# Kernel optimization log

Measured on AMD Instinct MI355X. Metric: run time of the kernel, lower is better.

The kernel has to match this reference:

```python
import jax, jax.numpy as jnp
import numpy as np

N, E, G = 20000, 400000, 200
IN, HID, OUT, H = 8, 64, 32, 4
EPS = 1e-5
NEG_SLOPE = 0.2


def _gatv2(x, src, dst, Wl, bl, Wr, br, att, bias, n, heads, c):
    # lin_l (source messages) and lin_r (target queries)
    xl = (x @ Wl + bl).reshape(n, heads, c)
    xr = (x @ Wr + br).reshape(n, heads, c)
    # per-edge GATv2 score: att . LeakyReLU(x_l[j] + x_r[i])
    e = jax.nn.leaky_relu(xl[src] + xr[dst], NEG_SLOPE)          # [E,H,C]
    score = jnp.einsum('ehc,hc->eh', e, att)                     # [E,H]
    # softmax over incoming edges of each target node
    m = jax.ops.segment_max(score, dst, num_segments=n)
    ex = jnp.exp(score - m[dst])
    den = jax.ops.segment_sum(ex, dst, num_segments=n)
    alpha = ex / den[dst]                                        # [E,H]
    out = jax.ops.segment_sum(alpha[:, :, None] * xl[src], dst, num_segments=n)
    return out.mean(axis=1) + bias                               # concat=False: head mean


def _layernorm(x, g, b):
    mu = x.mean(-1, keepdims=True)
    var = ((x - mu) ** 2).mean(-1, keepdims=True)
    return (x - mu) * jax.lax.rsqrt(var + EPS) * g + b


def setup_inputs() -> dict:
    key = jax.random.key(0)
    ks = jax.random.split(key, 16)
    s = 0.1
    inp = {
        'x': jax.random.normal(ks[0], (N, IN), jnp.float32),
        'edge_index': jax.random.randint(ks[1], (2, E), 0, N, jnp.int64 if jax.config.jax_enable_x64 else jnp.int32),
        'batch': jnp.sort(jax.random.randint(ks[2], (N,), 0, G)),
        'Wl1': jax.random.normal(ks[3], (IN, H * HID), jnp.float32) * s,
        'bl1': jnp.zeros((H * HID,), jnp.float32),
        'Wr1': jax.random.normal(ks[4], (IN, H * HID), jnp.float32) * s,
        'br1': jnp.zeros((H * HID,), jnp.float32),
        'att1': jax.random.normal(ks[5], (H, HID), jnp.float32) * s,
        'b1': jnp.zeros((HID,), jnp.float32),
        'ln1_g': jnp.ones((HID,), jnp.float32),
        'ln1_b': jnp.zeros((HID,), jnp.float32),
        'Wl2': jax.random.normal(ks[6], (HID, H * OUT), jnp.float32) * s,
        'bl2': jnp.zeros((H * OUT,), jnp.float32),
        'Wr2': jax.random.normal(ks[7], (HID, H * OUT), jnp.float32) * s,
        'br2': jnp.zeros((H * OUT,), jnp.float32),
        'att2': jax.random.normal(ks[8], (H, OUT), jnp.float32) * s,
        'b2': jnp.zeros((OUT,), jnp.float32),
        'ln2_g': jnp.ones((OUT,), jnp.float32),
        'ln2_b': jnp.zeros((OUT,), jnp.float32),
    }
    return inp


def reference(x, edge_index, batch, Wl1, bl1, Wr1, br1, att1, b1, ln1_g, ln1_b,
              Wl2, bl2, Wr2, br2, att2, b2, ln2_g, ln2_b):
    n = x.shape[0]
    loop = jnp.arange(n, dtype=edge_index.dtype)  # add_self_loops=True (PyG default)
    src = jnp.concatenate([edge_index[0], loop])
    dst = jnp.concatenate([edge_index[1], loop])

    h = _gatv2(x, src, dst, Wl1, bl1, Wr1, br1, att1, b1, n, H, HID)
    h = jax.nn.relu(_layernorm(h, ln1_g, ln1_b))
    h = _gatv2(h, src, dst, Wl2, bl2, Wr2, br2, att2, b2, n, H, OUT)
    h = jax.nn.relu(_layernorm(h, ln2_g, ln2_b))

    # global mean pool per graph
    cnt = jax.ops.segment_sum(jnp.ones((n,), h.dtype), batch, num_segments=G)
    pooled = jax.ops.segment_sum(h, batch, num_segments=G)
    return pooled / jnp.maximum(cnt, 1.0)[:, None]
```

## Files before the change

kernel.cpp:

```cpp
#include <hip/hip_runtime.h>
#include <math.h>
#include <stdint.h>

#define NEG_SLOPE 0.2f
#define LN_EPS 1e-5f

typedef __attribute__((ext_vector_type(8))) short short8;
typedef __attribute__((ext_vector_type(4))) float f32x4;

__device__ __forceinline__ uint32_t pack_bf2(float a, float b) {
  uint32_t ua = __float_as_uint(a);
  uint32_t ub = __float_as_uint(b);
  ua = (ua + 0x7fffu + ((ua >> 16) & 1u)) >> 16;
  ub = (ub + 0x7fffu + ((ub >> 16) & 1u)) & 0xffff0000u;
  return ua | ub;
}
__device__ __forceinline__ float2 unpack_bf2(uint32_t u) {
  return make_float2(__uint_as_float(u << 16), __uint_as_float(u & 0xffff0000u));
}
__device__ __forceinline__ uint16_t bf16_rne(float f) {
  uint32_t u = __float_as_uint(f);
  return (uint16_t)((u + 0x7fffu + ((u >> 16) & 1u)) >> 16);
}

__device__ __forceinline__ float row16_sum(float x) {
  x += __int_as_float(__builtin_amdgcn_mov_dpp(__float_as_int(x), 0xB1, 0xF, 0xF, true));
  x += __int_as_float(__builtin_amdgcn_mov_dpp(__float_as_int(x), 0x4E, 0xF, 0xF, true));
  x += __int_as_float(__builtin_amdgcn_mov_dpp(__float_as_int(x), 0x124, 0xF, 0xF, true));
  x += __int_as_float(__builtin_amdgcn_mov_dpp(__float_as_int(x), 0x128, 0xF, 0xF, true));
  return x;
}

__global__ __launch_bounds__(256) void gemm1_hist_kernel(
    const float* __restrict__ x,
    const float* __restrict__ Wl, const float* __restrict__ bl,
    const float* __restrict__ Wr, const float* __restrict__ br,
    uint32_t* __restrict__ xl1b, float* __restrict__ xr1, int N,
    const int* __restrict__ ei, int E, int* __restrict__ cnt) {
  int tid = threadIdx.x;
  int c2 = tid & 127;
  int which = tid >> 7;
  float wl0[8], wl1[8], wr0[8], wr1[8];
#pragma unroll
  for (int k = 0; k < 8; ++k) {
    wl0[k] = Wl[k * 256 + 2 * c2]; wl1[k] = Wl[k * 256 + 2 * c2 + 1];
    wr0[k] = Wr[k * 256 + 2 * c2]; wr1[k] = Wr[k * 256 + 2 * c2 + 1];
  }
  float bl0 = bl[2 * c2], bl1v = bl[2 * c2 + 1];
  float br0 = br[2 * c2], br1v = br[2 * c2 + 1];
  int npair = (N + 1) >> 1;
  for (int pr = blockIdx.x; pr < npair; pr += gridDim.x) {
    int n = pr * 2 + which;
    if (n >= N) continue;
    float4 xa = ((const float4*)x)[n * 2];
    float4 xb = ((const float4*)x)[n * 2 + 1];
    float xs[8] = {xa.x, xa.y, xa.z, xa.w, xb.x, xb.y, xb.z, xb.w};
    float al0 = bl0, al1 = bl1v, ar0 = br0, ar1 = br1v;
#pragma unroll
    for (int k = 0; k < 8; ++k) {
      al0 = fmaf(xs[k], wl0[k], al0); al1 = fmaf(xs[k], wl1[k], al1);
      ar0 = fmaf(xs[k], wr0[k], ar0); ar1 = fmaf(xs[k], wr1[k], ar1);
    }
    xl1b[(size_t)n * 128 + c2] = pack_bf2(al0, al1);
    ((float2*)xr1)[(size_t)n * 128 + c2] = make_float2(ar0, ar1);
  }
  int tot = E + N;
  for (int e = blockIdx.x * blockDim.x + tid; e < tot; e += gridDim.x * blockDim.x) {
    int dst = (e < E) ? ei[E + e] : (e - E);
    atomicAdd(&cnt[dst], 1);
  }
}

__global__ __launch_bounds__(1024) void scan_kernel(const int* __restrict__ cnt,
                                                    int* __restrict__ offs,
                                                    int* __restrict__ cursor, int n) {
  __shared__ int wsum[16];
  int tid = threadIdx.x;
  int lane = tid & 63, w = tid >> 6;
  int PER = (n + 1023) >> 10;
  int base = tid * PER;
  int s = 0;
  for (int j = 0; j < PER; ++j) {
    int idx = base + j;
    s += (idx < n) ? cnt[idx] : 0;
  }
  int inc = s;
#pragma unroll
  for (int d = 1; d < 64; d <<= 1) {
    int t = __shfl_up(inc, d, 64);
    if (lane >= d) inc += t;
  }
  if (lane == 63) wsum[w] = inc;
  __syncthreads();
  int wpre = 0;
  for (int j = 0; j < w; ++j) wpre += wsum[j];
  int run = wpre + inc - s;
  for (int j = 0; j < PER; ++j) {
    int idx = base + j;
    if (idx < n) {
      offs[idx] = run;
      cursor[idx] = run;
      run += cnt[idx];
    }
  }
  if (tid == 1023) offs[n] = run;
}

__global__ void scatter_kernel(const int* __restrict__ ei, int E, int N,
                               int* __restrict__ cursor, int* __restrict__ esrc,
                               const float* __restrict__ Wl2, const float* __restrict__ Wr2,
                               uint16_t* __restrict__ Wtb) {
  if (blockIdx.x < 64) {
    int idx = blockIdx.x * 256 + threadIdx.x;
    int c = idx >> 6, k = idx & 63;
    float v = (c < 128) ? Wl2[k * 128 + c] : Wr2[k * 128 + (c - 128)];
    Wtb[idx] = bf16_rne(v);
  }
  int e = blockIdx.x * blockDim.x + threadIdx.x;
  if (e >= E + N) return;
  int src, dst;
  if (e < E) { src = ei[e]; dst = ei[E + e]; }
  else       { src = e - E; dst = src; }
  int pos = atomicAdd(&cursor[dst], 1);
  esrc[pos] = src;
}

__global__ __launch_bounds__(256) void gemm2_mfma_kernel(
    const uint16_t* __restrict__ h1b,
    const uint16_t* __restrict__ Wtb,
    const float* __restrict__ bl, const float* __restrict__ br,
    uint32_t* __restrict__ xl2b, float* __restrict__ xr2, int N) {
  int lane = threadIdx.x & 63;
  int w = threadIdx.x >> 6;
  int c0 = w << 6;
  int l15 = lane & 15, l4 = lane >> 4;
  int node = (blockIdx.x << 4) + l15;
  int nodec = node < N ? node : N - 1;
  const short8* hrow = (const short8*)(h1b + (size_t)nodec * 64);
  short8 b0 = hrow[l4];
  short8 b1 = hrow[4 + l4];
  f32x4 acc[4] = {{0.f,0.f,0.f,0.f},{0.f,0.f,0.f,0.f},{0.f,0.f,0.f,0.f},{0.f,0.f,0.f,0.f}};
#pragma unroll
  for (int t = 0; t < 4; ++t) {
    int row = c0 + (t << 4) + l15;
    const short8* wrow = (const short8*)(Wtb + (size_t)row * 64);
    short8 a0 = wrow[l4];
    short8 a1 = wrow[4 + l4];
    acc[t] = __builtin_amdgcn_mfma_f32_16x16x32_bf16(a0, b0, acc[t], 0, 0, 0);
    acc[t] = __builtin_amdgcn_mfma_f32_16x16x32_bf16(a1, b1, acc[t], 0, 0, 0);
  }
  if (node >= N) return;
  if (c0 < 128) {
#pragma unroll
    for (int t = 0; t < 4; ++t) {
      int q0 = c0 + (t << 4) + (l4 << 2);
      float4 bb = *(const float4*)(bl + q0);
      uint2 pk;
      pk.x = pack_bf2(acc[t][0] + bb.x, acc[t][1] + bb.y);
      pk.y = pack_bf2(acc[t][2] + bb.z, acc[t][3] + bb.w);
      *(uint2*)(xl2b + (size_t)node * 64 + (q0 >> 1)) = pk;
    }
  } else {
#pragma unroll
    for (int t = 0; t < 4; ++t) {
      int q0 = (c0 - 128) + (t << 4) + (l4 << 2);
      float4 bb = *(const float4*)(br + q0);
      float4 v = make_float4(acc[t][0] + bb.x, acc[t][1] + bb.y,
                             acc[t][2] + bb.z, acc[t][3] + bb.w);
      *(float4*)(xr2 + (size_t)node * 128 + q0) = v;
    }
  }
}

__global__ __launch_bounds__(256) void attn1_kernel(
    const uint32_t* __restrict__ xl1b, const float* __restrict__ xr1,
    const float* __restrict__ att, const float* __restrict__ b1,
    const float* __restrict__ g, const float* __restrict__ be,
    const int* __restrict__ offs, const int* __restrict__ esrc,
    uint32_t* __restrict__ h1b, int N) {
  int lane = threadIdx.x & 63;
  int i = blockIdx.x * (blockDim.x >> 6) + (threadIdx.x >> 6);
  if (i >= N) return;
  int cq = lane & 15;
  const uint2* xlb = (const uint2*)xl1b;
  float4 attq = ((const float4*)att)[lane];
  float4 attn_ = make_float4(NEG_SLOPE * attq.x, NEG_SLOPE * attq.y,
                             NEG_SLOPE * attq.z, NEG_SLOPE * attq.w);
  float4 xrq = ((const float4*)xr1)[(size_t)i * 64 + lane];
  float dA = 0.f, aA0 = 0.f, aA1 = 0.f, aA2 = 0.f, aA3 = 0.f;
  float dB = 0.f, aB0 = 0.f, aB1 = 0.f, aB2 = 0.f, aB3 = 0.f;
  int beg = offs[i], end = offs[i + 1];
  int p = beg;

#define EDGE1(U, DD, A0, A1, A2, A3)                                           \
  {                                                                            \
    float2 e0 = unpack_bf2(U.x), e1 = unpack_bf2(U.y);                         \
    float t0 = e0.x + xrq.x, t1 = e0.y + xrq.y;                                \
    float t2 = e1.x + xrq.z, t3 = e1.y + xrq.w;                                \
    float sc = t0 * (t0 > 0.f ? attq.x : attn_.x);                             \
    sc = fmaf(t1, (t1 > 0.f ? attq.y : attn_.y), sc);                          \
    sc = fmaf(t2, (t2 > 0.f ? attq.z : attn_.z), sc);                          \
    sc = fmaf(t3, (t3 > 0.f ? attq.w : attn_.w), sc);                          \
    sc = row16_sum(sc);                                                        \
    float wgt = __expf(sc);                                                    \
    DD += wgt;                                                                 \
    A0 = fmaf(wgt, e0.x, A0); A1 = fmaf(wgt, e0.y, A1);                        \
    A2 = fmaf(wgt, e1.x, A2); A3 = fmaf(wgt, e1.y, A3);                        \
  }

  for (; p + 3 < end; p += 4) {
    int s0 = esrc[p], s1 = esrc[p + 1], s2 = esrc[p + 2], s3 = esrc[p + 3];
    uint2 u0 = xlb[(uint32_t)s0 * 64u + lane];
    uint2 u1 = xlb[(uint32_t)s1 * 64u + lane];
    uint2 u2 = xlb[(uint32_t)s2 * 64u + lane];
    uint2 u3 = xlb[(uint32_t)s3 * 64u + lane];
    EDGE1(u0, dA, aA0, aA1, aA2, aA3)
    EDGE1(u1, dB, aB0, aB1, aB2, aB3)
    EDGE1(u2, dA, aA0, aA1, aA2, aA3)
    EDGE1(u3, dB, aB0, aB1, aB2, aB3)
  }
  for (; p < end; ++p) {
    int s0 = esrc[p];
    uint2 u0 = xlb[(uint32_t)s0 * 64u + lane];
    EDGE1(u0, dA, aA0, aA1, aA2, aA3)
  }
#undef EDGE1

  float inv = 1.0f / (dA + dB);
  float v0 = (aA0 + aB0) * inv;
  float v1 = (aA1 + aB1) * inv;
  float v2 = (aA2 + aB2) * inv;
  float v3 = (aA3 + aB3) * inv;
  v0 += __shfl_xor(v0, 16, 64); v0 += __shfl_xor(v0, 32, 64);
  v1 += __shfl_xor(v1, 16, 64); v1 += __shfl_xor(v1, 32, 64);
  v2 += __shfl_xor(v2, 16, 64); v2 += __shfl_xor(v2, 32, 64);
  v3 += __shfl_xor(v3, 16, 64); v3 += __shfl_xor(v3, 32, 64);
  float4 b1q = ((const float4*)b1)[cq];
  v0 = 0.25f * v0 + b1q.x;
  v1 = 0.25f * v1 + b1q.y;
  v2 = 0.25f * v2 + b1q.z;
  v3 = 0.25f * v3 + b1q.w;
  float s1 = row16_sum(v0 + v1 + v2 + v3);
  float mu = s1 * (1.0f / 64.0f);
  float d0 = v0 - mu, d1 = v1 - mu, d2 = v2 - mu, d3 = v3 - mu;
  float s2 = row16_sum(d0 * d0 + d1 * d1 + d2 * d2 + d3 * d3);
  float rstd = rsqrtf(s2 * (1.0f / 64.0f) + LN_EPS);
  float4 gq = ((const float4*)g)[cq];
  float4 beq = ((const float4*)be)[cq];
  float y0 = fmaxf(fmaf(d0 * rstd, gq.x, beq.x), 0.f);
  float y1 = fmaxf(fmaf(d1 * rstd, gq.y, beq.y), 0.f);
  float y2 = fmaxf(fmaf(d2 * rstd, gq.z, beq.z), 0.f);
  float y3 = fmaxf(fmaf(d3 * rstd, gq.w, beq.w), 0.f);
  if (lane < 16) {
    uint2 pk;
    pk.x = pack_bf2(y0, y1);
    pk.y = pack_bf2(y2, y3);
    *(uint2*)(h1b + (size_t)i * 32 + cq * 2) = pk;
  }
}

__global__ __launch_bounds__(256) void attn2_kernel(
    const uint32_t* __restrict__ xl2b, const float* __restrict__ xr2,
    const float* __restrict__ att, const float* __restrict__ b2,
    const float* __restrict__ g, const float* __restrict__ be,
    const int* __restrict__ offs, const int* __restrict__ esrc,
    float* __restrict__ h2, int N) {
  int lane = threadIdx.x & 63;
  int i = blockIdx.x * (blockDim.x >> 6) + (threadIdx.x >> 6);
  if (i >= N) return;
  int cq = lane & 15;
  float2 attq = ((const float2*)att)[lane];
  float2 attn_ = make_float2(NEG_SLOPE * attq.x, NEG_SLOPE * attq.y);
  float2 xrq = ((const float2*)xr2)[(size_t)i * 64 + lane];
  float dA = 0.f, aA0 = 0.f, aA1 = 0.f;
  float dB = 0.f, aB0 = 0.f, aB1 = 0.f;
  int beg = offs[i], end = offs[i + 1];
  int p = beg;

#define EDGE2(U, DD, A0, A1)                                                   \
  {                                                                            \
    float2 e0 = unpack_bf2(U);                                                 \
    float t0 = e0.x + xrq.x, t1 = e0.y + xrq.y;                                \
    float sc = t0 * (t0 > 0.f ? attq.x : attn_.x);                             \
    sc = fmaf(t1, (t1 > 0.f ? attq.y : attn_.y), sc);                          \
    sc = row16_sum(sc);                                                        \
    float wgt = __expf(sc);                                                    \
    DD += wgt;                                                                 \
    A0 = fmaf(wgt, e0.x, A0); A1 = fmaf(wgt, e0.y, A1);                        \
  }

  for (; p + 3 < end; p += 4) {
    int s0 = esrc[p], s1 = esrc[p + 1], s2 = esrc[p + 2], s3 = esrc[p + 3];
    uint32_t u0 = xl2b[(uint32_t)s0 * 64u + lane];
    uint32_t u1 = xl2b[(uint32_t)s1 * 64u + lane];
    uint32_t u2 = xl2b[(uint32_t)s2 * 64u + lane];
    uint32_t u3 = xl2b[(uint32_t)s3 * 64u + lane];
    EDGE2(u0, dA, aA0, aA1)
    EDGE2(u1, dB, aB0, aB1)
    EDGE2(u2, dA, aA0, aA1)
    EDGE2(u3, dB, aB0, aB1)
  }
  for (; p < end; ++p) {
    int s0 = esrc[p];
    uint32_t u0 = xl2b[(uint32_t)s0 * 64u + lane];
    EDGE2(u0, dA, aA0, aA1)
  }
#undef EDGE2

  float inv = 1.0f / (dA + dB);
  float v0 = (aA0 + aB0) * inv;
  float v1 = (aA1 + aB1) * inv;
  v0 += __shfl_xor(v0, 16, 64); v0 += __shfl_xor(v0, 32, 64);
  v1 += __shfl_xor(v1, 16, 64); v1 += __shfl_xor(v1, 32, 64);
  float2 b2q = ((const float2*)b2)[cq];
  v0 = 0.25f * v0 + b2q.x;
  v1 = 0.25f * v1 + b2q.y;
  float s1 = row16_sum(v0 + v1);
  float mu = s1 * (1.0f / 32.0f);
  float d0 = v0 - mu, d1 = v1 - mu;
  float s2 = row16_sum(d0 * d0 + d1 * d1);
  float rstd = rsqrtf(s2 * (1.0f / 32.0f) + LN_EPS);
  float2 gq = ((const float2*)g)[cq];
  float2 beq = ((const float2*)be)[cq];
  float y0 = fmaxf(fmaf(d0 * rstd, gq.x, beq.x), 0.f);
  float y1 = fmaxf(fmaf(d1 * rstd, gq.y, beq.y), 0.f);
  if (lane < 16) ((float2*)h2)[(size_t)i * 16 + cq] = make_float2(y0, y1);
}

__global__ __launch_bounds__(256) void pool_kernel(const float* __restrict__ h2,
                                                   const int* __restrict__ batch,
                                                   float* __restrict__ out, int N) {
  int gidx = blockIdx.x;
  int a = 0, b = N;
  while (a < b) { int m = (a + b) >> 1; if (batch[m] < gidx) a = m + 1; else b = m; }
  int lo = a;
  b = N;
  while (a < b) { int m = (a + b) >> 1; if (batch[m] < gidx + 1) a = m + 1; else b = m; }
  int hi = a;
  int c = threadIdx.x & 31, r = threadIdx.x >> 5;
  float s = 0.f;
  for (int n = lo + r; n < hi; n += 8) s += h2[(size_t)n * 32 + c];
  __shared__ float buf[256];
  buf[threadIdx.x] = s;
  __syncthreads();
  if (threadIdx.x < 128) buf[threadIdx.x] += buf[threadIdx.x + 128];
  __syncthreads();
  if (threadIdx.x < 64) buf[threadIdx.x] += buf[threadIdx.x + 64];
  __syncthreads();
  if (threadIdx.x < 32) {
    float v = buf[threadIdx.x] + buf[threadIdx.x + 32];
    int cnt = hi - lo;
    out[gidx * 32 + threadIdx.x] = v / (float)(cnt > 0 ? cnt : 1);
  }
}

extern "C" void kernel_launch(void* const* d_in, const int* in_sizes, int n_in,
                              void* d_out, int out_size, void* d_ws, size_t ws_size,
                              hipStream_t stream) {
  const float* x    = (const float*)d_in[0];
  const int*   ei   = (const int*)d_in[1];
  const int*   batch= (const int*)d_in[2];
  const float* Wl1  = (const float*)d_in[3];
  const float* bl1  = (const float*)d_in[4];
  const float* Wr1  = (const float*)d_in[5];
  const float* br1  = (const float*)d_in[6];
  const float* att1 = (const float*)d_in[7];
  const float* b1   = (const float*)d_in[8];
  const float* ln1g = (const float*)d_in[9];
  const float* ln1b = (const float*)d_in[10];
  const float* Wl2  = (const float*)d_in[11];
  const float* bl2  = (const float*)d_in[12];
  const float* Wr2  = (const float*)d_in[13];
  const float* br2  = (const float*)d_in[14];
  const float* att2 = (const float*)d_in[15];
  const float* b2   = (const float*)d_in[16];
  const float* ln2g = (const float*)d_in[17];
  const float* ln2b = (const float*)d_in[18];

  int N = in_sizes[0] / 8;
  int E = in_sizes[1] / 2;
  int G = out_size / 32;

  char* ws = (char*)d_ws;
  size_t off = 0;
  auto alloc = [&](size_t bytes) -> void* {
    void* p = (void*)(ws + off);
    off += (bytes + 255) & ~(size_t)255;
    return p;
  };
  int*      cnt    = (int*)alloc((size_t)N * 4);
  int*      offs   = (int*)alloc((size_t)(N + 1) * 4);
  int*      cursor = (int*)alloc((size_t)N * 4);
  int*      esrc   = (int*)alloc((size_t)(E + N) * 4);
  uint32_t* xl1b   = (uint32_t*)alloc((size_t)N * 128 * 4);
  float*    xr1    = (float*)alloc((size_t)N * 256 * 4);
  uint32_t* h1b    = (uint32_t*)alloc((size_t)N * 64 * 2);
  uint16_t* Wtb    = (uint16_t*)alloc((size_t)256 * 64 * 2);
  uint32_t* xl2b   = (uint32_t*)alloc((size_t)N * 64 * 4);
  float*    xr2    = (float*)alloc((size_t)N * 128 * 4);
  float*    h2     = (float*)alloc((size_t)N * 32 * 4);

  hipMemsetAsync(cnt, 0, (size_t)N * 4, stream);

  int tot = E + N;
  gemm1_hist_kernel<<<2048, 256, 0, stream>>>(x, Wl1, bl1, Wr1, br1, xl1b, xr1, N,
                                              ei, E, cnt);
  scan_kernel<<<1, 1024, 0, stream>>>(cnt, offs, cursor, N);
  scatter_kernel<<<(tot + 255) / 256, 256, 0, stream>>>(ei, E, N, cursor, esrc,
                                                        Wl2, Wr2, Wtb);

  attn1_kernel<<<(N + 3) / 4, 256, 0, stream>>>(xl1b, xr1, att1, b1, ln1g, ln1b,
                                                offs, esrc, h1b, N);
  gemm2_mfma_kernel<<<(N + 15) / 16, 256, 0, stream>>>((const uint16_t*)h1b, Wtb, bl2, br2,
                                                       xl2b, xr2, N);
  attn2_kernel<<<(N + 3) / 4, 256, 0, stream>>>(xl2b, xr2, att2, b2, ln2g, ln2b,
                                                offs, esrc, h2, N);

  pool_kernel<<<G, 256, 0, stream>>>(h2, batch, (float*)d_out, N);
}
```

Before: 173.6 us.

## Use abs-based LeakyReLU with exp2, scalarize edge indices, replace memset with kernel

```diff
diff --git a/kernel.cpp b/kernel.cpp
--- a/kernel.cpp
+++ b/kernel.cpp
@@ -29,6 +29,11 @@
   x += __int_as_float(__builtin_amdgcn_mov_dpp(__float_as_int(x), 0x124, 0xF, 0xF, true));
   x += __int_as_float(__builtin_amdgcn_mov_dpp(__float_as_int(x), 0x128, 0xF, 0xF, true));
   return x;
+}
+
+__global__ void zero_kernel(int* __restrict__ p, int n) {
+  int i = blockIdx.x * blockDim.x + threadIdx.x;
+  if (i < n) p[i] = 0;
 }
 
 __global__ __launch_bounds__(256) void gemm1_hist_kernel(
@@ -178,14 +183,15 @@
     const float* __restrict__ g, const float* __restrict__ be,
     const int* __restrict__ offs, const int* __restrict__ esrc,
     uint32_t* __restrict__ h1b, int N) {
+  const float L2E = 1.4426950408889634f;
   int lane = threadIdx.x & 63;
   int i = blockIdx.x * (blockDim.x >> 6) + (threadIdx.x >> 6);
   if (i >= N) return;
   int cq = lane & 15;
   const uint2* xlb = (const uint2*)xl1b;
   float4 attq = ((const float4*)att)[lane];
-  float4 attn_ = make_float4(NEG_SLOPE * attq.x, NEG_SLOPE * attq.y,
-                             NEG_SLOPE * attq.z, NEG_SLOPE * attq.w);
+  float4 a4 = make_float4(0.4f * L2E * attq.x, 0.4f * L2E * attq.y,
+                          0.4f * L2E * attq.z, 0.4f * L2E * attq.w);
   float4 xrq = ((const float4*)xr1)[(size_t)i * 64 + lane];
   float dA = 0.f, aA0 = 0.f, aA1 = 0.f, aA2 = 0.f, aA3 = 0.f;
   float dB = 0.f, aB0 = 0.f, aB1 = 0.f, aB2 = 0.f, aB3 = 0.f;
@@ -197,31 +203,38 @@
     float2 e0 = unpack_bf2(U.x), e1 = unpack_bf2(U.y);                         \
     float t0 = e0.x + xrq.x, t1 = e0.y + xrq.y;                                \
     float t2 = e1.x + xrq.z, t3 = e1.y + xrq.w;                                \
-    float sc = t0 * (t0 > 0.f ? attq.x : attn_.x);                             \
-    sc = fmaf(t1, (t1 > 0.f ? attq.y : attn_.y), sc);                          \
-    sc = fmaf(t2, (t2 > 0.f ? attq.z : attn_.z), sc);                          \
-    sc = fmaf(t3, (t3 > 0.f ? attq.w : attn_.w), sc);                          \
+    float u0 = fmaf(1.5f, t0, fabsf(t0));                                      \
+    float u1 = fmaf(1.5f, t1, fabsf(t1));                                      \
+    float u2 = fmaf(1.5f, t2, fabsf(t2));                                      \
+    float u3 = fmaf(1.5f, t3, fabsf(t3));                                      \
+    float sc = a4.x * u0;                                                      \
+    sc = fmaf(a4.y, u1, sc);                                                   \
+    sc = fmaf(a4.z, u2, sc);                                                   \
+    sc = fmaf(a4.w, u3, sc);                                                   \
     sc = row16_sum(sc);                                                        \
-    float wgt = __expf(sc);                                                    \
+    float wgt = exp2f(sc);                                                     \
     DD += wgt;                                                                 \
     A0 = fmaf(wgt, e0.x, A0); A1 = fmaf(wgt, e0.y, A1);                        \
     A2 = fmaf(wgt, e1.x, A2); A3 = fmaf(wgt, e1.y, A3);                        \
   }
 
   for (; p + 3 < end; p += 4) {
-    int s0 = esrc[p], s1 = esrc[p + 1], s2 = esrc[p + 2], s3 = esrc[p + 3];
-    uint2 u0 = xlb[(uint32_t)s0 * 64u + lane];
-    uint2 u1 = xlb[(uint32_t)s1 * 64u + lane];
-    uint2 u2 = xlb[(uint32_t)s2 * 64u + lane];
-    uint2 u3 = xlb[(uint32_t)s3 * 64u + lane];
+    int s0 = __builtin_amdgcn_readfirstlane(esrc[p]);
+    int s1 = __builtin_amdgcn_readfirstlane(esrc[p + 1]);
+    int s2 = __builtin_amdgcn_readfirstlane(esrc[p + 2]);
+    int s3 = __builtin_amdgcn_readfirstlane(esrc[p + 3]);
+    uint2 u0 = (xlb + (size_t)s0 * 64)[lane];
+    uint2 u1 = (xlb + (size_t)s1 * 64)[lane];
+    uint2 u2 = (xlb + (size_t)s2 * 64)[lane];
+    uint2 u3 = (xlb + (size_t)s3 * 64)[lane];
     EDGE1(u0, dA, aA0, aA1, aA2, aA3)
     EDGE1(u1, dB, aB0, aB1, aB2, aB3)
     EDGE1(u2, dA, aA0, aA1, aA2, aA3)
     EDGE1(u3, dB, aB0, aB1, aB2, aB3)
   }
   for (; p < end; ++p) {
-    int s0 = esrc[p];
-    uint2 u0 = xlb[(uint32_t)s0 * 64u + lane];
+    int s0 = __builtin_amdgcn_readfirstlane(esrc[p]);
+    uint2 u0 = (xlb + (size_t)s0 * 64)[lane];
     EDGE1(u0, dA, aA0, aA1, aA2, aA3)
   }
 #undef EDGE1
@@ -265,12 +278,13 @@
     const float* __restrict__ g, const float* __restrict__ be,
     const int* __restrict__ offs, const int* __restrict__ esrc,
     float* __restrict__ h2, int N) {
+  const float L2E = 1.4426950408889634f;
   int lane = threadIdx.x & 63;
   int i = blockIdx.x * (blockDim.x >> 6) + (threadIdx.x >> 6);
   if (i >= N) return;
   int cq = lane & 15;
   float2 attq = ((const float2*)att)[lane];
-  float2 attn_ = make_float2(NEG_SLOPE * attq.x, NEG_SLOPE * attq.y);
+  float2 a4 = make_float2(0.4f * L2E * attq.x, 0.4f * L2E * attq.y);
   float2 xrq = ((const float2*)xr2)[(size_t)i * 64 + lane];
   float dA = 0.f, aA0 = 0.f, aA1 = 0.f;
   float dB = 0.f, aB0 = 0.f, aB1 = 0.f;
@@ -281,28 +295,32 @@
   {                                                                            \
     float2 e0 = unpack_bf2(U);                                                 \
     float t0 = e0.x + xrq.x, t1 = e0.y + xrq.y;                                \
-    float sc = t0 * (t0 > 0.f ? attq.x : attn_.x);                             \
-    sc = fmaf(t1, (t1 > 0.f ? attq.y : attn_.y), sc);                          \
+    float u0 = fmaf(1.5f, t0, fabsf(t0));                                      \
+    float u1 = fmaf(1.5f, t1, fabsf(t1));                                      \
+    float sc = fmaf(a4.y, u1, a4.x * u0);                                      \
     sc = row16_sum(sc);                                                        \
-    float wgt = __expf(sc);                                                    \
+    float wgt = exp2f(sc);                                                     \
     DD += wgt;                                                                 \
     A0 = fmaf(wgt, e0.x, A0); A1 = fmaf(wgt, e0.y, A1);                        \
   }
 
   for (; p + 3 < end; p += 4) {
-    int s0 = esrc[p], s1 = esrc[p + 1], s2 = esrc[p + 2], s3 = esrc[p + 3];
-    uint32_t u0 = xl2b[(uint32_t)s0 * 64u + lane];
-    uint32_t u1 = xl2b[(uint32_t)s1 * 64u + lane];
-    uint32_t u2 = xl2b[(uint32_t)s2 * 64u + lane];
-    uint32_t u3 = xl2b[(uint32_t)s3 * 64u + lane];
+    int s0 = __builtin_amdgcn_readfirstlane(esrc[p]);
+    int s1 = __builtin_amdgcn_readfirstlane(esrc[p + 1]);
+    int s2 = __builtin_amdgcn_readfirstlane(esrc[p + 2]);
+    int s3 = __builtin_amdgcn_readfirstlane(esrc[p + 3]);
+    uint32_t u0 = (xl2b + (size_t)s0 * 64)[lane];
+    uint32_t u1 = (xl2b + (size_t)s1 * 64)[lane];
+    uint32_t u2 = (xl2b + (size_t)s2 * 64)[lane];
+    uint32_t u3 = (xl2b + (size_t)s3 * 64)[lane];
     EDGE2(u0, dA, aA0, aA1)
     EDGE2(u1, dB, aB0, aB1)
     EDGE2(u2, dA, aA0, aA1)
     EDGE2(u3, dB, aB0, aB1)
   }
   for (; p < end; ++p) {
-    int s0 = esrc[p];
-    uint32_t u0 = xl2b[(uint32_t)s0 * 64u + lane];
+    int s0 = __builtin_amdgcn_readfirstlane(esrc[p]);
+    uint32_t u0 = (xl2b + (size_t)s0 * 64)[lane];
     EDGE2(u0, dA, aA0, aA1)
   }
 #undef EDGE2
@@ -400,9 +418,8 @@
   float*    xr2    = (float*)alloc((size_t)N * 128 * 4);
   float*    h2     = (float*)alloc((size_t)N * 32 * 4);
 
-  hipMemsetAsync(cnt, 0, (size_t)N * 4, stream);
-
   int tot = E + N;
+  zero_kernel<<<(N + 255) / 256, 256, 0, stream>>>(cnt, N);
   gemm1_hist_kernel<<<2048, 256, 0, stream>>>(x, Wl1, bl1, Wr1, br1, xl1b, xr1, N,
                                               ei, E, cnt);
   scan_kernel<<<1, 1024, 0, stream>>>(cnt, offs, cursor, N);
```

Result: no change. 175.8 us (+1.3%).
